# Performance work log

Hardware: AMD Instinct MI355X
Metric: run time of the kernel (lower is better)

## Reference

```python
import jax, jax.numpy as jnp
import numpy as np

N, F, P, NT = 4096, 256, 5, 5  # agents, feat dim, n_persona, n_time_steps
EPS = 1e-8


def setup_inputs() -> dict:
    key = jax.random.key(0)
    ks = jax.random.split(key, 7)
    attributes = jax.random.normal(ks[0], (N, F), dtype=jnp.float32)
    edges = (jax.random.uniform(ks[1], (N, N)) < 0.01).astype(jnp.float32)
    persona = jax.random.uniform(ks[2], (NT, N, P), dtype=jnp.float32)
    T = jax.random.uniform(ks[3], (P,), dtype=jnp.float32) * 0.5 + 0.5  # keep temperature away from 0
    e = jax.random.uniform(ks[4], (P,), dtype=jnp.float32) + 0.5
    r = jax.random.uniform(ks[5], (P,), dtype=jnp.float32)
    W = jax.random.uniform(ks[6], (P,), dtype=jnp.float32) + 0.5
    return {"attributes": attributes, "edges": edges, "persona": persona,
            "T": T, "e": e, "r": r, "W": W, "times": 2}


def reference(attributes, edges, persona, T, e, r, W, times):
    p = persona[times]                      # [N, P] persona weights at this time step
    msg = edges @ attributes                # [N, F] message passing, shared across personas

    def body(acc, xs):
        idx, Ti, ei, ri, Wi, pi = xs        # pi: [N]
        feat = ri * attributes + (msg * Wi) * (1.0 - ri)          # [N, F]
        nf = feat / jnp.sqrt(jnp.sum(feat * feat, axis=1, keepdims=True))  # row L2 norm
        x = jnp.exp((nf @ nf.T) / (Ti + EPS)) * ei                 # [N, N]
        x = x / (jnp.max(x) + EPS)                                 # min-max scale (min=0)
        # (1 - exp(-2v)) / (1 + exp(-2v)) == tanh(v)
        tc = jnp.tanh(x) * pi[None, :]                              # column persona gating
        # i == 0 initializes edges_prob with tc, every i adds row-gated tc
        acc = acc + tc * pi[:, None] + jnp.where(idx == 0, 1.0, 0.0) * tc
        return acc, None

    acc0 = jnp.zeros((N, N), dtype=jnp.float32)
    out, _ = jax.lax.scan(body, acc0, (jnp.arange(P), T, e, r, W, p.T))
    return out
```

## Files before the change

kernel.cpp:

```cpp
#include <hip/hip_runtime.h>
#include <hip/hip_bf16.h>

#define N 4096
#define F 256
#define P 5
#define EPSV 1e-8f
#define BK 32
#define NSTEP (F / BK)
#define NTRI 2080
#define GRIDSZ 768
#define DDEG 12
#define NC (DDEG + 1)

typedef __attribute__((ext_vector_type(8))) short bf16x8;
typedef __attribute__((ext_vector_type(4))) float f32x4;
typedef __attribute__((ext_vector_type(2))) float f32x2;

__device__ __forceinline__ f32x4 mfma16(bf16x8 a, bf16x8 b, f32x4 c) {
    return __builtin_amdgcn_mfma_f32_16x16x32_bf16(a, b, c, 0, 0, 0);
}

__device__ __forceinline__ void gload16(const void* src, const char* ldsdst) {
    __builtin_amdgcn_global_load_lds(
        (const __attribute__((address_space(1))) void*)src,
        (__attribute__((address_space(3))) void*)ldsdst, 16, 0, 0);
}

__device__ __forceinline__ f32x2 sp(float x) { return (f32x2){x, x}; }

__global__ __launch_bounds__(256, 8) void prep_kernel(
    const float* __restrict__ E, const float* __restrict__ A,
    const float* __restrict__ persona,
    const float* __restrict__ Tt, const float* __restrict__ ee,
    const float* __restrict__ rr, const float* __restrict__ Ww,
    const int* __restrict__ times,
    __hip_bfloat16* __restrict__ Abf, __hip_bfloat16* __restrict__ Mbf,
    float* __restrict__ qsoa, float* __restrict__ cstg, int* __restrict__ ctr) {
    __shared__ int cnt;
    __shared__ int list[1024];
    const int a = blockIdx.x;
    const int t = threadIdx.x;
    if (t == 0) cnt = 0;
    __syncthreads();
    const float4* erow = (const float4*)(E + (size_t)a * N);
    for (int b = t; b < N / 4; b += 256) {
        const float4 v = erow[b];
        if (v.x != 0.f) list[atomicAdd(&cnt, 1)] = 4 * b;
        if (v.y != 0.f) list[atomicAdd(&cnt, 1)] = 4 * b + 1;
        if (v.z != 0.f) list[atomicAdd(&cnt, 1)] = 4 * b + 2;
        if (v.w != 0.f) list[atomicAdd(&cnt, 1)] = 4 * b + 3;
    }
    __syncthreads();
    const int c = cnt;
    float s0 = 0.f, s1 = 0.f, s2 = 0.f, s3 = 0.f;
    float s4 = 0.f, s5 = 0.f, s6 = 0.f, s7 = 0.f;
    int j = 0;
    for (; j + 8 <= c; j += 8) {
        s0 += A[(size_t)list[j] * F + t];
        s1 += A[(size_t)list[j + 1] * F + t];
        s2 += A[(size_t)list[j + 2] * F + t];
        s3 += A[(size_t)list[j + 3] * F + t];
        s4 += A[(size_t)list[j + 4] * F + t];
        s5 += A[(size_t)list[j + 5] * F + t];
        s6 += A[(size_t)list[j + 6] * F + t];
        s7 += A[(size_t)list[j + 7] * F + t];
    }
    for (; j < c; ++j) s0 += A[(size_t)list[j] * F + t];
    const float mv = ((s0 + s1) + (s2 + s3)) + ((s4 + s5) + (s6 + s7));
    const float av = A[(size_t)a * F + t];
    Abf[(size_t)a * F + t] = __float2bfloat16(av);
    Mbf[(size_t)a * F + t] = __float2bfloat16(mv);

    float paa = av * av, pam = av * mv, pmm = mv * mv;
    #pragma unroll
    for (int o = 32; o > 0; o >>= 1) {
        paa += __shfl_down(paa, o);
        pam += __shfl_down(pam, o);
        pmm += __shfl_down(pmm, o);
    }
    __shared__ float s[3][4];
    const int wid = t >> 6;
    if ((t & 63) == 0) { s[0][wid] = paa; s[1][wid] = pam; s[2][wid] = pmm; }
    __syncthreads();
    if (t < P) {
        const float naa = s[0][0] + s[0][1] + s[0][2] + s[0][3];
        const float nam = s[1][0] + s[1][1] + s[1][2] + s[1][3];
        const float nmm = s[2][0] + s[2][1] + s[2][2] + s[2][3];
        const float Ti = Tt[t], ei = ee[t], ri = rr[t], Wi = Ww[t];
        const float wb = (1.f - ri) * Wi;
        const float n2 = ri * ri * naa + 2.f * ri * wb * nam + wb * wb * nmm;
        const float rn = rsqrtf(n2);
        const float p = persona[(size_t)(*times) * (size_t)N * P + (size_t)a * P + t];
        qsoa[(t * 4 + 0) * N + a] = ri * rn;
        qsoa[(t * 4 + 1) * N + a] = wb * rn;
        qsoa[(t * 4 + 2) * N + a] = p;
        qsoa[(t * 4 + 3) * N + a] = p + (t == 0 ? 1.f : 0.f);
        if (a == 0) {
            const float kk = 1.f / (Ti + EPSV);
            const float scf = ei / (ei * __expf(kk) + EPSV);
            float ch[NC];
            #pragma unroll
            for (int j2 = 0; j2 < NC; ++j2) ch[j2] = 0.f;
            for (int m = 0; m < 32; ++m) {
                const float th = 3.14159265358979323846f * (m + 0.5f) / 32.f;
                const float c1 = __cosf(th);
                const float x = scf * __expf(kk * 1.05f * c1);
                const float e2 = __expf(2.f * x);
                const float fm = 1.f - 2.f / (e2 + 1.f);
                float cjm1 = 1.f, cj = c1;
                ch[0] += fm;
                ch[1] += fm * c1;
                #pragma unroll
                for (int j2 = 2; j2 < NC; ++j2) {
                    const float cn = 2.f * c1 * cj - cjm1;
                    ch[j2] += fm * cn;
                    cjm1 = cj;
                    cj = cn;
                }
            }
            #pragma unroll
            for (int j2 = 0; j2 < NC; ++j2) ch[j2] *= (j2 == 0 ? 1.f : 2.f) / 32.f;
            float mono[NC], Tp[NC], Tc[NC], Tn[NC];
            const float is = 1.f / 1.05f;
            #pragma unroll
            for (int k2 = 0; k2 < NC; ++k2) {
                mono[k2] = 0.f; Tp[k2] = 0.f; Tc[k2] = 0.f; Tn[k2] = 0.f;
            }
            Tp[0] = 1.f;
            Tc[1] = is;
            #pragma unroll
            for (int k2 = 0; k2 < NC; ++k2) mono[k2] += ch[0] * Tp[k2] + ch[1] * Tc[k2];
            for (int j2 = 2; j2 < NC; ++j2) {
                #pragma unroll
                for (int k2 = 0; k2 < NC; ++k2)
                    Tn[k2] = 2.f * is * (k2 ? Tc[k2 - 1] : 0.f) - Tp[k2];
                #pragma unroll
                for (int k2 = 0; k2 < NC; ++k2) mono[k2] += ch[j2] * Tn[k2];
                #pragma unroll
                for (int k2 = 0; k2 < NC; ++k2) { Tp[k2] = Tc[k2]; Tc[k2] = Tn[k2]; }
            }
            #pragma unroll
            for (int k2 = 0; k2 < NC; ++k2) cstg[t * NC + k2] = mono[k2];
        }
    }
    if (a == 0 && t == 0) *ctr = GRIDSZ;
}

__global__ __launch_bounds__(512) void gram_kernel(
    const __hip_bfloat16* __restrict__ Abf, const __hip_bfloat16* __restrict__ Mbf,
    const float* __restrict__ qsoa, const float* __restrict__ cstg,
    int* __restrict__ ctr, float* __restrict__ out) {
    __shared__ __align__(16) char smem[43280];
    __shared__ int snext;

    const int t = threadIdx.x;
    const int lane = t & 63;
    const int w = t >> 6;
    const int wr = w >> 1;
    const int wc = w & 1;

    const int sslot = (lane & 3) ^ ((lane >> 3) & 3);
    const int srowoff = (w & 1) * 32 + (lane >> 2);
    const int ldsp = (w >> 1) * 4096 + (w & 1) * 2048;
    const __hip_bfloat16* smat = ((w >> 1) & 1) ? Mbf : Abf;

    const int frow = lane & 15;
    const int fg = lane >> 4;
    const int jr = fg << 2;
    const int rdslot = (fg ^ ((frow >> 1) & 3)) << 4;
    const int aoff = (wr * 16 + frow) * 64 + rdslot;
    const int coff0 = (wc * 32 + frow) * 64 + rdslot;
    const int coff1 = (wc * 32 + 16 + frow) * 64 + rdslot;

    const float* qlr = (const float*)(smem + 32768);
    const float* qlc = (const float*)(smem + 37888);
    const float* cfs = (const float*)(smem + 43008);

    int raw = blockIdx.x;
    while (raw < NTRI) {
        const int bid = (raw & 7) * 260 + (raw >> 3);
        int bx = (int)((sqrtf(8.f * (float)bid + 1.f) - 1.f) * 0.5f);
        while ((bx + 1) * (bx + 2) / 2 <= bid) ++bx;
        while (bx * (bx + 1) / 2 > bid) --bx;
        const int by = bid - bx * (bx + 1) / 2;
        const int row0 = by << 6, col0 = bx << 6;

        const int sbase = (w < 4) ? row0 : col0;
        const __hip_bfloat16* psrc =
            smat + (size_t)(sbase + srowoff) * F + sslot * 8;

        #define STAGE(b, ks)  do {                                        \
            const char* lb_ = smem + (b) * 16384 + ldsp;                  \
            gload16(psrc + (ks), lb_);                                    \
            gload16(psrc + (ks) + 16 * F, lb_ + 1024);                    \
        } while (0)

        __syncthreads();
        STAGE(0, 0);
        if (w == 0) {
            #pragma unroll
            for (int it = 0; it < 5; ++it)
                gload16(qsoa + (it * 4 + (lane >> 4)) * N + row0 + (lane & 15) * 4,
                        smem + 32768 + it * 1024);
        } else if (w == 1) {
            #pragma unroll
            for (int it = 0; it < 5; ++it)
                gload16(qsoa + (it * 4 + (lane >> 4)) * N + col0 + (lane & 15) * 4,
                        smem + 37888 + it * 1024);
        } else if (w == 2) {
            if (lane < 17) gload16(cstg + lane * 4, smem + 43008);
        }
        if (t == 0) snext = atomicAdd(ctr, 1);
        __syncthreads();

        f32x4 acc[4][2];
        #pragma unroll
        for (int g = 0; g < 4; ++g)
            #pragma unroll
            for (int n = 0; n < 2; ++n) acc[g][n] = (f32x4){0.f, 0.f, 0.f, 0.f};

        for (int s = 0; s < NSTEP; ++s) {
            const int b = s & 1;
            if (s + 1 < NSTEP) STAGE(b ^ 1, (s + 1) * BK);
            const char* base = smem + b * 16384;
            const bf16x8 aA = *(const bf16x8*)(base + aoff);
            const bf16x8 aM = *(const bf16x8*)(base + 4096 + aoff);
            const bf16x8 bA0 = *(const bf16x8*)(base + 8192 + coff0);
            const bf16x8 bA1 = *(const bf16x8*)(base + 8192 + coff1);
            const bf16x8 bM0 = *(const bf16x8*)(base + 12288 + coff0);
            const bf16x8 bM1 = *(const bf16x8*)(base + 12288 + coff1);
            acc[0][0] = mfma16(aA, bA0, acc[0][0]);
            acc[0][1] = mfma16(aA, bA1, acc[0][1]);
            acc[1][0] = mfma16(aA, bM0, acc[1][0]);
            acc[1][1] = mfma16(aA, bM1, acc[1][1]);
            acc[2][0] = mfma16(aM, bA0, acc[2][0]);
            acc[2][1] = mfma16(aM, bA1, acc[2][1]);
            acc[3][0] = mfma16(aM, bM0, acc[3][0]);
            acc[3][1] = mfma16(aM, bM1, acc[3][1]);
            if (s + 1 < NSTEP) __syncthreads();
        }

        f32x2 o1[2][2], o2[2][2];
        #pragma unroll
        for (int n = 0; n < 2; ++n)
            #pragma unroll
            for (int jp = 0; jp < 2; ++jp) { o1[n][jp] = sp(0.f); o2[n][jp] = sp(0.f); }

        #pragma unroll
        for (int i = 0; i < P; ++i) {
            const int ib = i * 256;
            float cf[NC];
            #pragma unroll
            for (int k = 0; k < NC; ++k) cf[k] = cfs[i * NC + k];
            float cA[2], cB[2], cP0[2], cP1[2];
            #pragma unroll
            for (int n = 0; n < 2; ++n) {
                const int cr = wc * 32 + n * 16 + frow;
                cA[n]  = qlc[ib + cr];
                cB[n]  = qlc[ib + 64 + cr];
                cP0[n] = qlc[ib + 128 + cr];
                cP1[n] = qlc[ib + 192 + cr];
            }
            #pragma unroll
            for (int jp = 0; jp < 2; ++jp) {
                const int rrw = wr * 16 + jr + jp * 2;
                const f32x2 rA  = *(const f32x2*)&qlr[ib + rrw];
                const f32x2 rB  = *(const f32x2*)&qlr[ib + 64 + rrw];
                const f32x2 rP0 = *(const f32x2*)&qlr[ib + 128 + rrw];
                const f32x2 rP1 = *(const f32x2*)&qlr[ib + 192 + rrw];
                #pragma unroll
                for (int n = 0; n < 2; ++n) {
                    const f32x2 aAA = (f32x2){acc[0][n][2 * jp], acc[0][n][2 * jp + 1]};
                    const f32x2 aAM = (f32x2){acc[1][n][2 * jp], acc[1][n][2 * jp + 1]};
                    const f32x2 aMA = (f32x2){acc[2][n][2 * jp], acc[2][n][2 * jp + 1]};
                    const f32x2 aMM = (f32x2){acc[3][n][2 * jp], acc[3][n][2 * jp + 1]};
                    const f32x2 h0 = rA * aAA + rB * aMA;
                    const f32x2 h1 = rA * aAM + rB * aMM;
                    const f32x2 g2 = h0 * sp(cA[n]) + h1 * sp(cB[n]);
                    f32x2 f2 = sp(cf[DDEG]);
                    #pragma unroll
                    for (int k = DDEG - 1; k >= 0; --k) f2 = f2 * g2 + sp(cf[k]);
                    o1[n][jp] += (f2 * rP1) * sp(cP0[n]);
                    o2[n][jp] += (f2 * rP0) * sp(cP1[n]);
                }
            }
        }

        #pragma unroll
        for (int jp = 0; jp < 2; ++jp)
            #pragma unroll
            for (int cc = 0; cc < 2; ++cc) {
                const int gr = row0 + wr * 16 + jr + jp * 2 + cc;
                #pragma unroll
                for (int n = 0; n < 2; ++n) {
                    const int gc = col0 + wc * 32 + n * 16 + frow;
                    out[(size_t)gr * N + gc] = o1[n][jp][cc];
                }
            }
        if (by != bx) {
            #pragma unroll
            for (int jp = 0; jp < 2; ++jp)
                #pragma unroll
                for (int cc = 0; cc < 2; ++cc) {
                    const int gr = row0 + wr * 16 + jr + jp * 2 + cc;
                    #pragma unroll
                    for (int n = 0; n < 2; ++n) {
                        const int gc = col0 + wc * 32 + n * 16 + frow;
                        out[(size_t)gc * N + gr] = o2[n][jp][cc];
                    }
                }
        }
        raw = snext;
        #undef STAGE
    }
}

extern "C" void kernel_launch(void* const* d_in, const int* in_sizes, int n_in,
                              void* d_out, int out_size, void* d_ws, size_t ws_size,
                              hipStream_t stream) {
    const float* A = (const float*)d_in[0];
    const float* E = (const float*)d_in[1];
    const float* persona = (const float*)d_in[2];
    const float* T = (const float*)d_in[3];
    const float* e = (const float*)d_in[4];
    const float* r = (const float*)d_in[5];
    const float* W = (const float*)d_in[6];
    const int* times = (const int*)d_in[7];
    float* out = (float*)d_out;

    char* ws = (char*)d_ws;
    __hip_bfloat16* Abf = (__hip_bfloat16*)ws;
    __hip_bfloat16* Mbf = (__hip_bfloat16*)(ws + (2 << 20));
    float* qsoa = (float*)(ws + (4 << 20));
    float* cstg = (float*)(ws + (4 << 20) + 5 * 4 * N * 4);
    int* ctr = (int*)(ws + (4 << 20) + 5 * 4 * N * 4 + 512);

    prep_kernel<<<N, 256, 0, stream>>>(E, A, persona, T, e, r, W, times,
                                       Abf, Mbf, qsoa, cstg, ctr);
    gram_kernel<<<GRIDSZ, 512, 0, stream>>>(Abf, Mbf, qsoa, cstg, ctr, out);
}
```

Measured before the change: 89.67 us.

## Load row operands directly to registers and triple-buffer column tiles in LDS

```diff
diff --git a/kernel.cpp b/kernel.cpp
--- a/kernel.cpp
+++ b/kernel.cpp
@@ -146,11 +146,17 @@
     if (a == 0 && t == 0) *ctr = GRIDSZ;
 }
 
+#define RAWBAR() do {                                   \
+    __builtin_amdgcn_sched_barrier(0);                  \
+    __builtin_amdgcn_s_barrier();                       \
+    __builtin_amdgcn_sched_barrier(0);                  \
+} while (0)
+
 __global__ __launch_bounds__(512) void gram_kernel(
     const __hip_bfloat16* __restrict__ Abf, const __hip_bfloat16* __restrict__ Mbf,
     const float* __restrict__ qsoa, const float* __restrict__ cstg,
     int* __restrict__ ctr, float* __restrict__ out) {
-    __shared__ __align__(16) char smem[43280];
+    __shared__ __align__(16) char smem[35088];
     __shared__ int snext;
 
     const int t = threadIdx.x;
@@ -159,22 +165,22 @@
     const int wr = w >> 1;
     const int wc = w & 1;
 
+    const int pA = w >> 2;
     const int sslot = (lane & 3) ^ ((lane >> 3) & 3);
-    const int srowoff = (w & 1) * 32 + (lane >> 2);
-    const int ldsp = (w >> 1) * 4096 + (w & 1) * 2048;
-    const __hip_bfloat16* smat = ((w >> 1) & 1) ? Mbf : Abf;
+    const int csrow = (w & 3) * 16 + (lane >> 2);
+    const __hip_bfloat16* cmat = pA ? Mbf : Abf;
+    const int ldsp = pA * 4096 + (w & 3) * 1024;
 
     const int frow = lane & 15;
     const int fg = lane >> 4;
     const int jr = fg << 2;
     const int rdslot = (fg ^ ((frow >> 1) & 3)) << 4;
-    const int aoff = (wr * 16 + frow) * 64 + rdslot;
     const int coff0 = (wc * 32 + frow) * 64 + rdslot;
     const int coff1 = (wc * 32 + 16 + frow) * 64 + rdslot;
 
-    const float* qlr = (const float*)(smem + 32768);
-    const float* qlc = (const float*)(smem + 37888);
-    const float* cfs = (const float*)(smem + 43008);
+    const float* qlr = (const float*)(smem + 24576);
+    const float* qlc = (const float*)(smem + 29696);
+    const float* cfs = (const float*)(smem + 34816);
 
     int raw = blockIdx.x;
     while (raw < NTRI) {
@@ -185,33 +191,38 @@
         const int by = bid - bx * (bx + 1) / 2;
         const int row0 = by << 6, col0 = bx << 6;
 
-        const int sbase = (w < 4) ? row0 : col0;
-        const __hip_bfloat16* psrc =
-            smat + (size_t)(sbase + srowoff) * F + sslot * 8;
-
-        #define STAGE(b, ks)  do {                                        \
-            const char* lb_ = smem + (b) * 16384 + ldsp;                  \
-            gload16(psrc + (ks), lb_);                                    \
-            gload16(psrc + (ks) + 16 * F, lb_ + 1024);                    \
-        } while (0)
-
-        __syncthreads();
+        const __hip_bfloat16* csrc =
+            cmat + (size_t)(col0 + csrow) * F + sslot * 8;
+        const __hip_bfloat16* prA =
+            Abf + (size_t)(row0 + wr * 16 + frow) * F + fg * 8;
+        const __hip_bfloat16* prM =
+            Mbf + (size_t)(row0 + wr * 16 + frow) * F + fg * 8;
+
+        #define STAGE(b, ks) gload16(csrc + (ks), smem + (b) * 8192 + ldsp)
+
+        RAWBAR();
+
         STAGE(0, 0);
+        STAGE(1, 32);
+        bf16x8 rowA[2], rowM[2];
+        rowA[0] = *(const bf16x8*)(prA);
+        rowM[0] = *(const bf16x8*)(prM);
         if (w == 0) {
             #pragma unroll
             for (int it = 0; it < 5; ++it)
                 gload16(qsoa + (it * 4 + (lane >> 4)) * N + row0 + (lane & 15) * 4,
-                        smem + 32768 + it * 1024);
+                        smem + 24576 + it * 1024);
         } else if (w == 1) {
             #pragma unroll
             for (int it = 0; it < 5; ++it)
                 gload16(qsoa + (it * 4 + (lane >> 4)) * N + col0 + (lane & 15) * 4,
-                        smem + 37888 + it * 1024);
+                        smem + 29696 + it * 1024);
         } else if (w == 2) {
-            if (lane < 17) gload16(cstg + lane * 4, smem + 43008);
+            if (lane < 17) gload16(cstg + lane * 4, smem + 34816);
         }
         if (t == 0) snext = atomicAdd(ctr, 1);
-        __syncthreads();
+        asm volatile("s_waitcnt vmcnt(3)" ::: "memory");
+        RAWBAR();
 
         f32x4 acc[4][2];
         #pragma unroll
@@ -219,25 +230,34 @@
             #pragma unroll
             for (int n = 0; n < 2; ++n) acc[g][n] = (f32x4){0.f, 0.f, 0.f, 0.f};
 
+        #pragma unroll
         for (int s = 0; s < NSTEP; ++s) {
-            const int b = s & 1;
-            if (s + 1 < NSTEP) STAGE(b ^ 1, (s + 1) * BK);
-            const char* base = smem + b * 16384;
-            const bf16x8 aA = *(const bf16x8*)(base + aoff);
-            const bf16x8 aM = *(const bf16x8*)(base + 4096 + aoff);
-            const bf16x8 bA0 = *(const bf16x8*)(base + 8192 + coff0);
-            const bf16x8 bA1 = *(const bf16x8*)(base + 8192 + coff1);
-            const bf16x8 bM0 = *(const bf16x8*)(base + 12288 + coff0);
-            const bf16x8 bM1 = *(const bf16x8*)(base + 12288 + coff1);
-            acc[0][0] = mfma16(aA, bA0, acc[0][0]);
-            acc[0][1] = mfma16(aA, bA1, acc[0][1]);
-            acc[1][0] = mfma16(aA, bM0, acc[1][0]);
-            acc[1][1] = mfma16(aA, bM1, acc[1][1]);
-            acc[2][0] = mfma16(aM, bA0, acc[2][0]);
-            acc[2][1] = mfma16(aM, bA1, acc[2][1]);
-            acc[3][0] = mfma16(aM, bM0, acc[3][0]);
-            acc[3][1] = mfma16(aM, bM1, acc[3][1]);
-            if (s + 1 < NSTEP) __syncthreads();
+            if (s + 2 < NSTEP) STAGE((s + 2) % 3, (s + 2) * BK);
+            if (s + 1 < NSTEP) {
+                rowA[(s + 1) & 1] = *(const bf16x8*)(prA + (s + 1) * BK);
+                rowM[(s + 1) & 1] = *(const bf16x8*)(prM + (s + 1) * BK);
+            }
+            const char* base = smem + (s % 3) * 8192;
+            const bf16x8 bA0 = *(const bf16x8*)(base + coff0);
+            const bf16x8 bA1 = *(const bf16x8*)(base + coff1);
+            const bf16x8 bM0 = *(const bf16x8*)(base + 4096 + coff0);
+            const bf16x8 bM1 = *(const bf16x8*)(base + 4096 + coff1);
+            acc[0][0] = mfma16(rowA[s & 1], bA0, acc[0][0]);
+            acc[0][1] = mfma16(rowA[s & 1], bA1, acc[0][1]);
+            acc[1][0] = mfma16(rowA[s & 1], bM0, acc[1][0]);
+            acc[1][1] = mfma16(rowA[s & 1], bM1, acc[1][1]);
+            acc[2][0] = mfma16(rowM[s & 1], bA0, acc[2][0]);
+            acc[2][1] = mfma16(rowM[s & 1], bA1, acc[2][1]);
+            acc[3][0] = mfma16(rowM[s & 1], bM0, acc[3][0]);
+            acc[3][1] = mfma16(rowM[s & 1], bM1, acc[3][1]);
+            if (s + 1 < NSTEP) {
+                if (s + 2 < NSTEP) {
+                    asm volatile("s_waitcnt vmcnt(3)" ::: "memory");
+                } else {
+                    asm volatile("s_waitcnt vmcnt(2)" ::: "memory");
+                }
+                RAWBAR();
+            }
         }
 
         f32x2 o1[2][2], o2[2][2];
```

Result: slower. 100.7 us (+12.3%).
